# Optimization experiments

Measured on AMD Instinct MI355X. Metric: run time of the kernel, lower is better.

## Reference

```python
import jax, jax.numpy as jnp
import numpy as np

C_M, C_H, C_Z = 256, 32, 128
LN_EPS = 1e-5
MASK_EPS = 1e-8


def setup_inputs() -> dict:
    key = jax.random.key(0)
    ks = jax.random.split(key, 8)
    B, N, L = 1, 128, 256
    m = jax.random.normal(ks[0], (B, N, L, C_M), dtype=jnp.float32)
    msa_mask = jnp.ones((B, N, L), dtype=jnp.float32)
    # parameters
    ln_gamma = jnp.ones((C_M,), dtype=jnp.float32)
    ln_beta = jnp.zeros((C_M,), dtype=jnp.float32)
    sa = 1.0 / np.sqrt(C_M)
    Wa = jax.random.uniform(ks[1], (C_M, C_H), jnp.float32, -sa, sa)
    ba = jax.random.uniform(ks[2], (C_H,), jnp.float32, -sa, sa)
    Wb = jax.random.uniform(ks[3], (C_M, C_H), jnp.float32, -sa, sa)
    bb = jax.random.uniform(ks[4], (C_H,), jnp.float32, -sa, sa)
    so = 1.0 / np.sqrt(C_H * C_H)
    Wo = jax.random.uniform(ks[5], (C_H * C_H, C_Z), jnp.float32, -so, so)
    bo = jax.random.uniform(ks[6], (C_Z,), jnp.float32, -so, so)
    return {"m": m, "msa_mask": msa_mask, "ln_gamma": ln_gamma, "ln_beta": ln_beta,
            "Wa": Wa, "ba": ba, "Wb": Wb, "bb": bb, "Wo": Wo, "bo": bo}


def reference(m, msa_mask, ln_gamma, ln_beta, Wa, ba, Wb, bb, Wo, bo):
    B, N, L, _ = m.shape
    # LayerNorm over c_m
    mu = jnp.mean(m, axis=-1, keepdims=True)
    var = jnp.mean(jnp.square(m - mu), axis=-1, keepdims=True)
    x = (m - mu) * jax.lax.rsqrt(var + LN_EPS) * ln_gamma + ln_beta
    a = x @ Wa + ba                       # [B,N,L,c_h]
    b = x @ Wb + bb                       # [B,N,L,c_h]
    mk = msa_mask[..., None]
    a = a * mk
    b = b * mk
    # outer product mean over MSA depth: [B,L,L,c_h,c_h]
    outer = jnp.einsum('bnic,bnjd->bijcd', a, b)
    pair_mask = jnp.einsum('bni,bnj->bij', msa_mask, msa_mask)
    outer = outer / (pair_mask[..., None, None] + MASK_EPS)
    outer = outer.reshape(B, L, L, -1)    # [B,L,L,c_h*c_h]
    z_update = outer @ Wo + bo            # [B,L,L,c_z]
    return z_update
```

## Files before the change

kernel.cpp:

```cpp
#include <hip/hip_runtime.h>
#include <hip/hip_bf16.h>


typedef __attribute__((ext_vector_type(8))) short bf8_t;
typedef __attribute__((ext_vector_type(4))) float f32x4;

__device__ __forceinline__ unsigned short f2bf(float f) {
    unsigned int u = __float_as_uint(f);
    u += 0x7fffu + ((u >> 16) & 1u);
    return (unsigned short)(u >> 16);
}
__device__ __forceinline__ unsigned int pack2(float a, float b) {
    return (unsigned int)f2bf(a) | ((unsigned int)f2bf(b) << 16);
}

__device__ __forceinline__ void cp16_async(const void* g, void* l) {
    __builtin_amdgcn_global_load_lds(
        (const __attribute__((address_space(1))) unsigned int*)g,
        (__attribute__((address_space(3))) unsigned int*)l, 16, 0, 0);
}

__global__ __launch_bounds__(256) void k_prep(const float* __restrict__ Wa,
                                              const float* __restrict__ Wb,
                                              unsigned short* __restrict__ WTb) {
    int u = blockIdx.x * 256 + threadIdx.x;
    int h = u >> 8, c = u & 255;
    float v = (h < 32) ? Wa[c * 32 + h] : Wb[c * 32 + (h - 32)];
    WTb[u] = f2bf(v);
}

__global__ __launch_bounds__(256) void k_ln_proj(
    const float* __restrict__ gm, const float* __restrict__ gmask,
    const float* __restrict__ gamma, const float* __restrict__ beta,
    const unsigned short* __restrict__ WTb,
    const float* __restrict__ ba, const float* __restrict__ bb,
    const float* __restrict__ Wo,
    unsigned short* __restrict__ aT, unsigned short* __restrict__ bT,
    unsigned short* __restrict__ W2, float* __restrict__ pmr)
{
    const int tid = threadIdx.x;
    const int tail = (int)blockIdx.x - 2048;
    if (tail >= 0) {
        if (tail < 512) {
            int u = tail * 256 + tid;
            int k = u >> 7, z = u & 127;
            int c = k >> 5, d = k & 31;
            int kp = d * 32 + c;
            int dst = (((z >> 4) * 32 + (kp >> 5)) * 16 + (z & 15)) * 32
                      + ((kp >> 3) & 3) * 8 + (kp & 7);
            W2[dst] = f2bf(Wo[u]);
        } else {
            int u = (tail - 512) * 256 + tid;
            int i = u >> 8, j = u & 255;
            float s = 0.f;
            #pragma unroll 8
            for (int n = 0; n < 128; n++)
                s += gmask[n * 256 + i] * gmask[n * 256 + j];
            pmr[u] = 1.f / (s + 1e-8f);
        }
        return;
    }

    __shared__ __align__(16) unsigned short xlb[16 * 256];
    __shared__ float vl[16 * 64];
    const int lane = tid & 63, w = tid >> 6;
    const int l = blockIdx.x & 255, n0 = ((int)blockIdx.x >> 8) << 4;

    const float4 g4  = ((const float4*)gamma)[lane];
    const float4 be4 = ((const float4*)beta)[lane];

    #pragma unroll
    for (int j = 0; j < 4; j++) {
        int row = w * 4 + j;
        int n = n0 + row;
        float4 v = ((const float4*)(gm + ((size_t)n * 256 + l) * 256))[lane];
        float s = v.x + v.y + v.z + v.w;
        float q = v.x * v.x + v.y * v.y + v.z * v.z + v.w * v.w;
        #pragma unroll
        for (int off = 1; off < 64; off <<= 1) {
            s += __shfl_xor(s, off);
            q += __shfl_xor(q, off);
        }
        float mean = s * (1.f / 256.f);
        float var = fmaxf(q * (1.f / 256.f) - mean * mean, 0.f);
        float rstd = rsqrtf(var + 1e-5f);
        float x0 = (v.x - mean) * rstd * g4.x + be4.x;
        float x1 = (v.y - mean) * rstd * g4.y + be4.y;
        float x2 = (v.z - mean) * rstd * g4.z + be4.z;
        float x3 = (v.w - mean) * rstd * g4.w + be4.w;
        int c8s = lane ^ ((row & 7) << 1);
        *(uint2*)((char*)xlb + row * 512 + (c8s << 3)) =
            make_uint2(pack2(x0, x1), pack2(x2, x3));
    }
    __syncthreads();

    const int kg = lane >> 4, r16 = lane & 15;
    const int h = w * 16 + r16;
    f32x4 acc = {0.f, 0.f, 0.f, 0.f};
    #pragma unroll
    for (int ks = 0; ks < 8; ks++) {
        int c8 = ks * 8 + kg * 2;
        bf8_t af = *(const bf8_t*)((char*)xlb + r16 * 512 +
                                   ((c8 ^ ((r16 & 7) << 1)) << 3));
        bf8_t wf = *(const bf8_t*)(WTb + (size_t)h * 256 + ks * 32 + kg * 8);
        acc = __builtin_amdgcn_mfma_f32_16x16x32_bf16(af, wf, acc, 0, 0, 0);
    }
    float bias = (h < 32) ? ba[h] : bb[h - 32];
    #pragma unroll
    for (int r = 0; r < 4; r++) {
        int nrow = kg * 4 + r;
        float mk = gmask[(size_t)(n0 + nrow) * 256 + l];
        vl[nrow * 64 + h] = (acc[r] + bias) * mk;
    }
    __syncthreads();

    if (tid < 128) {
        int row = tid >> 1, half = tid & 1;
        int hh = row & 31;
        unsigned short* dst = (row < 32) ? aT : bT;
        unsigned int pk[4];
        #pragma unroll
        for (int jj = 0; jj < 4; jj++)
            pk[jj] = pack2(vl[(half * 8 + 2 * jj) * 64 + row],
                           vl[(half * 8 + 2 * jj + 1) * 64 + row]);
        *(uint4*)(dst + ((size_t)l * 32 + hh) * 128 + n0 + half * 8) =
            make_uint4(pk[0], pk[1], pk[2], pk[3]);
    }
}

__global__ __launch_bounds__(512, 3) void k_outer(
    const unsigned short* __restrict__ aT, const unsigned short* __restrict__ bT,
    const unsigned short* __restrict__ W2, const float* __restrict__ pmr,
    const float* __restrict__ bo, float* __restrict__ out)
{
    __shared__ __align__(16) char smem[65536];
    const int tid = threadIdx.x, lane = tid & 63, w = tid >> 6;
    const int wr = w >> 1, wc = w & 1;
    const int tj = blockIdx.x & 63, ti = blockIdx.x >> 6;
    const int kg = lane >> 4, r16 = lane & 15;

    f32x4 acc[4][4];
    #pragma unroll
    for (int mt = 0; mt < 4; mt++)
        #pragma unroll
        for (int nt = 0; nt < 4; nt++)
            acc[mt][nt] = (f32x4){0.f, 0.f, 0.f, 0.f};

    const uint4* gA = (const uint4*)(aT + (size_t)ti * 32768);
    const uint4* gB = (const uint4*)(bT + (size_t)tj * 16384);

    #pragma unroll
    for (int half = 0; half < 2; half++) {
        #pragma unroll
        for (int t = 0; t < 4; t++) {
            int q = w * 256 + t * 64 + lane;
            int row = q >> 3, c = q & 7;
            cp16_async(gA + row * 16 + half * 8 + (c ^ (row & 7)),
                       smem + ((w * 256 + t * 64) << 4));
        }
        #pragma unroll
        for (int t = 0; t < 2; t++) {
            int q = w * 128 + t * 64 + lane;
            int row = q >> 3, c = q & 7;
            cp16_async(gB + row * 16 + half * 8 + (c ^ (row & 7)),
                       smem + 32768 + ((w * 128 + t * 64) << 4));
        }
        __syncthreads();

        #pragma unroll
        for (int ks2 = 0; ks2 < 2; ks2++) {
            int ch = ks2 * 4 + kg;
            bf8_t af[4];
            #pragma unroll
            for (int mt = 0; mt < 4; mt++) {
                int mm = wr * 64 + mt * 16 + r16;
                af[mt] = *(const bf8_t*)(smem + mm * 128 + ((ch ^ (mm & 7)) << 4));
            }
            #pragma unroll
            for (int nt = 0; nt < 4; nt++) {
                int nn = wc * 64 + nt * 16 + r16;
                bf8_t bfr = *(const bf8_t*)(smem + 32768 + nn * 128 +
                                            ((ch ^ (nn & 7)) << 4));
                #pragma unroll
                for (int mt = 0; mt < 4; mt++)
                    acc[mt][nt] = __builtin_amdgcn_mfma_f32_16x16x32_bf16(
                        af[mt], bfr, acc[mt][nt], 0, 0, 0);
            }
        }
        __syncthreads();
    }

    unsigned short* O2b = (unsigned short*)smem;
    #pragma unroll
    for (int mt = 0; mt < 4; mt++) {
        int mmb = wr * 64 + mt * 16 + kg * 4;
        #pragma unroll
        for (int nt = 0; nt < 4; nt++) {
            int nn = wc * 64 + nt * 16 + r16;
            int p  = ((mmb >> 5) << 2) | (nn >> 5);
            int k2 = ((nn & 31) << 5) | (mmb & 31);
            int c2 = k2 >> 3;
            int pc = c2 ^ ((c2 >> 3) & 7) ^ (p & 7);
            *(uint2*)(O2b + p * 1024 + pc * 8 + (k2 & 7)) =
                make_uint2(pack2(acc[mt][nt][0], acc[mt][nt][1]),
                           pack2(acc[mt][nt][2], acc[mt][nt][3]));
        }
    }
    __syncthreads();

    f32x4 acc2[2];
    acc2[0] = (f32x4){0.f, 0.f, 0.f, 0.f};
    acc2[1] = (f32x4){0.f, 0.f, 0.f, 0.f};
    const unsigned short* O2r = O2b + r16 * 1024;
    const int psw = r16 & 7;
    const unsigned short* wz = W2 + (size_t)w * 16384 + r16 * 32 + kg * 8;

#define W2LD(x) (*(const bf8_t*)(wz + (x) * 512))
    bf8_t w0 = W2LD(0), w1 = W2LD(1), w2 = W2LD(2), w3 = W2LD(3);
    bf8_t w4 = W2LD(4), w5 = W2LD(5), w6 = W2LD(6), w7 = W2LD(7);

#define S2_ITER(s, wreg, PF)                                                  \
    {                                                                         \
        bf8_t wcur = wreg;                                                    \
        PF;                                                                   \
        int c2 = (s) * 4 + kg;                                                \
        int pc = c2 ^ ((c2 >> 3) & 7) ^ psw;                                  \
        bf8_t a0 = *(const bf8_t*)(O2r + pc * 8);                             \
        bf8_t a1 = *(const bf8_t*)(O2r + 16384 + pc * 8);                     \
        acc2[0] = __builtin_amdgcn_mfma_f32_16x16x32_bf16(a0, wcur, acc2[0],  \
                                                          0, 0, 0);           \
        acc2[1] = __builtin_amdgcn_mfma_f32_16x16x32_bf16(a1, wcur, acc2[1],  \
                                                          0, 0, 0);           \
    }

    #pragma unroll
    for (int sb = 0; sb < 4; sb++) {
        S2_ITER(sb * 8 + 0, w0, if (sb < 3) w0 = W2LD(sb * 8 + 8))
        S2_ITER(sb * 8 + 1, w1, if (sb < 3) w1 = W2LD(sb * 8 + 9))
        S2_ITER(sb * 8 + 2, w2, if (sb < 3) w2 = W2LD(sb * 8 + 10))
        S2_ITER(sb * 8 + 3, w3, if (sb < 3) w3 = W2LD(sb * 8 + 11))
        S2_ITER(sb * 8 + 4, w4, if (sb < 3) w4 = W2LD(sb * 8 + 12))
        S2_ITER(sb * 8 + 5, w5, if (sb < 3) w5 = W2LD(sb * 8 + 13))
        S2_ITER(sb * 8 + 6, w6, if (sb < 3) w6 = W2LD(sb * 8 + 14))
        S2_ITER(sb * 8 + 7, w7, if (sb < 3) w7 = W2LD(sb * 8 + 15))
    }
#undef S2_ITER
#undef W2LD

    const int i0 = ti * 8, j0 = tj * 4;
    const int z = w * 16 + r16;
    const float boz = bo[z];
    #pragma unroll
    for (int mt = 0; mt < 2; mt++)
        #pragma unroll
        for (int r = 0; r < 4; r++) {
            int p = mt * 16 + kg * 4 + r;
            int i = i0 + (p >> 2), j = j0 + (p & 3);
            float recip = pmr[i * 256 + j];
            out[((size_t)(i * 256 + j)) * 128 + z] = acc2[mt][r] * recip + boz;
        }
}

extern "C" void kernel_launch(void* const* d_in, const int* in_sizes, int n_in,
                              void* d_out, int out_size, void* d_ws, size_t ws_size,
                              hipStream_t stream)
{
    const float* m    = (const float*)d_in[0];
    const float* mask = (const float*)d_in[1];
    const float* gam  = (const float*)d_in[2];
    const float* bet  = (const float*)d_in[3];
    const float* Wa   = (const float*)d_in[4];
    const float* ba   = (const float*)d_in[5];
    const float* Wb   = (const float*)d_in[6];
    const float* bb   = (const float*)d_in[7];
    const float* Wo   = (const float*)d_in[8];
    const float* bo   = (const float*)d_in[9];
    float* out = (float*)d_out;

    unsigned short* aT  = (unsigned short*)d_ws;
    unsigned short* bT  = aT + 8192 * 128;
    unsigned short* W2  = bT + 8192 * 128;
    unsigned short* WTb = W2 + 128 * 1024;
    float* pmr = (float*)(WTb + 64 * 256);

    k_prep   <<<  64, 256, 0, stream>>>(Wa, Wb, WTb);
    k_ln_proj<<<2816, 256, 0, stream>>>(m, mask, gam, bet, WTb, ba, bb, Wo,
                                        aT, bT, W2, pmr);
    k_outer  <<<2048, 512, 0, stream>>>(aT, bT, W2, pmr, bo, out);
}
```

Measured before the change: 157.5 us.

## Enlarge outer-product tile to 8x8 residue pairs and split output GEMM by K halves

The k_outer block tile grows from 8x4 to 8x8 residue pairs, halving the grid to 1024 blocks. Each block now loads a full 256-row B tile, and each warp accumulates 8x4 MFMA tiles. Because the larger outer-product result no longer fits in shared memory, it is staged through LDS in two K halves that feed the Wo projection, with an extra barrier between them. This is meant to halve redundant Wo (W2) loads per output and improve reuse, at the cost of doubled accumulator registers and occupancy lowered to 2 blocks per CU.

```diff
diff --git a/kernel.cpp b/kernel.cpp
--- a/kernel.cpp
+++ b/kernel.cpp
@@ -128,26 +128,26 @@
     }
 }
 
-__global__ __launch_bounds__(512, 3) void k_outer(
+__global__ __launch_bounds__(512, 2) void k_outer(
     const unsigned short* __restrict__ aT, const unsigned short* __restrict__ bT,
     const unsigned short* __restrict__ W2, const float* __restrict__ pmr,
     const float* __restrict__ bo, float* __restrict__ out)
 {
     __shared__ __align__(16) char smem[65536];
     const int tid = threadIdx.x, lane = tid & 63, w = tid >> 6;
-    const int wr = w >> 1, wc = w & 1;
-    const int tj = blockIdx.x & 63, ti = blockIdx.x >> 6;
+    const int wr = w >> 2, wc = w & 3;
+    const int tj = blockIdx.x & 31, ti = blockIdx.x >> 5;
     const int kg = lane >> 4, r16 = lane & 15;
 
-    f32x4 acc[4][4];
-    #pragma unroll
-    for (int mt = 0; mt < 4; mt++)
+    f32x4 acc[8][4];
+    #pragma unroll
+    for (int mt = 0; mt < 8; mt++)
         #pragma unroll
         for (int nt = 0; nt < 4; nt++)
             acc[mt][nt] = (f32x4){0.f, 0.f, 0.f, 0.f};
 
     const uint4* gA = (const uint4*)(aT + (size_t)ti * 32768);
-    const uint4* gB = (const uint4*)(bT + (size_t)tj * 16384);
+    const uint4* gB = (const uint4*)(bT + (size_t)tj * 32768);
 
     #pragma unroll
     for (int half = 0; half < 2; half++) {
@@ -156,24 +156,24 @@
             int q = w * 256 + t * 64 + lane;
             int row = q >> 3, c = q & 7;
             cp16_async(gA + row * 16 + half * 8 + (c ^ (row & 7)),
-                       smem + ((w * 256 + t * 64) << 4));
-        }
-        #pragma unroll
-        for (int t = 0; t < 2; t++) {
-            int q = w * 128 + t * 64 + lane;
+                       smem + (q << 4) - (lane << 4));
+        }
+        #pragma unroll
+        for (int t = 0; t < 4; t++) {
+            int q = w * 256 + t * 64 + lane;
             int row = q >> 3, c = q & 7;
             cp16_async(gB + row * 16 + half * 8 + (c ^ (row & 7)),
-                       smem + 32768 + ((w * 128 + t * 64) << 4));
+                       smem + 32768 + (q << 4) - (lane << 4));
         }
         __syncthreads();
 
         #pragma unroll
         for (int ks2 = 0; ks2 < 2; ks2++) {
             int ch = ks2 * 4 + kg;
-            bf8_t af[4];
+            bf8_t af[8];
             #pragma unroll
-            for (int mt = 0; mt < 4; mt++) {
-                int mm = wr * 64 + mt * 16 + r16;
+            for (int mt = 0; mt < 8; mt++) {
+                int mm = wr * 128 + mt * 16 + r16;
                 af[mt] = *(const bf8_t*)(smem + mm * 128 + ((ch ^ (mm & 7)) << 4));
             }
             #pragma unroll
@@ -182,7 +182,7 @@
                 bf8_t bfr = *(const bf8_t*)(smem + 32768 + nn * 128 +
                                             ((ch ^ (nn & 7)) << 4));
                 #pragma unroll
-                for (int mt = 0; mt < 4; mt++)
+                for (int mt = 0; mt < 8; mt++)
                     acc[mt][nt] = __builtin_amdgcn_mfma_f32_16x16x32_bf16(
                         af[mt], bfr, acc[mt][nt], 0, 0, 0);
             }
@@ -191,27 +191,9 @@
     }
 
     unsigned short* O2b = (unsigned short*)smem;
-    #pragma unroll
-    for (int mt = 0; mt < 4; mt++) {
-        int mmb = wr * 64 + mt * 16 + kg * 4;
-        #pragma unroll
-        for (int nt = 0; nt < 4; nt++) {
-            int nn = wc * 64 + nt * 16 + r16;
-            int p  = ((mmb >> 5) << 2) | (nn >> 5);
-            int k2 = ((nn & 31) << 5) | (mmb & 31);
-            int c2 = k2 >> 3;
-            int pc = c2 ^ ((c2 >> 3) & 7) ^ (p & 7);
-            *(uint2*)(O2b + p * 1024 + pc * 8 + (k2 & 7)) =
-                make_uint2(pack2(acc[mt][nt][0], acc[mt][nt][1]),
-                           pack2(acc[mt][nt][2], acc[mt][nt][3]));
-        }
-    }
-    __syncthreads();
-
-    f32x4 acc2[2];
-    acc2[0] = (f32x4){0.f, 0.f, 0.f, 0.f};
-    acc2[1] = (f32x4){0.f, 0.f, 0.f, 0.f};
-    const unsigned short* O2r = O2b + r16 * 1024;
+    f32x4 acc2[4];
+    #pragma unroll
+    for (int q = 0; q < 4; q++) acc2[q] = (f32x4){0.f, 0.f, 0.f, 0.f};
     const int psw = r16 & 7;
     const unsigned short* wz = W2 + (size_t)w * 16384 + r16 * 32 + kg * 8;
 
@@ -219,45 +201,78 @@
     bf8_t w0 = W2LD(0), w1 = W2LD(1), w2 = W2LD(2), w3 = W2LD(3);
     bf8_t w4 = W2LD(4), w5 = W2LD(5), w6 = W2LD(6), w7 = W2LD(7);
 
-#define S2_ITER(s, wreg, PF)                                                  \
+#define S2_ITER(sl, wreg, PF)                                                 \
     {                                                                         \
         bf8_t wcur = wreg;                                                    \
         PF;                                                                   \
-        int c2 = (s) * 4 + kg;                                                \
-        int pc = c2 ^ ((c2 >> 3) & 7) ^ psw;                                  \
-        bf8_t a0 = *(const bf8_t*)(O2r + pc * 8);                             \
-        bf8_t a1 = *(const bf8_t*)(O2r + 16384 + pc * 8);                     \
+        int c2h = (sl) * 4 + kg;                                              \
+        int pcs = c2h ^ ((c2h >> 3) & 7) ^ psw;                               \
+        const unsigned short* ar = O2b + r16 * 512 + pcs * 8;                 \
+        bf8_t a0 = *(const bf8_t*)(ar);                                       \
+        bf8_t a1 = *(const bf8_t*)(ar + 16 * 512);                            \
+        bf8_t a2 = *(const bf8_t*)(ar + 32 * 512);                            \
+        bf8_t a3 = *(const bf8_t*)(ar + 48 * 512);                            \
         acc2[0] = __builtin_amdgcn_mfma_f32_16x16x32_bf16(a0, wcur, acc2[0],  \
                                                           0, 0, 0);           \
         acc2[1] = __builtin_amdgcn_mfma_f32_16x16x32_bf16(a1, wcur, acc2[1],  \
                                                           0, 0, 0);           \
-    }
-
-    #pragma unroll
-    for (int sb = 0; sb < 4; sb++) {
-        S2_ITER(sb * 8 + 0, w0, if (sb < 3) w0 = W2LD(sb * 8 + 8))
-        S2_ITER(sb * 8 + 1, w1, if (sb < 3) w1 = W2LD(sb * 8 + 9))
-        S2_ITER(sb * 8 + 2, w2, if (sb < 3) w2 = W2LD(sb * 8 + 10))
-        S2_ITER(sb * 8 + 3, w3, if (sb < 3) w3 = W2LD(sb * 8 + 11))
-        S2_ITER(sb * 8 + 4, w4, if (sb < 3) w4 = W2LD(sb * 8 + 12))
-        S2_ITER(sb * 8 + 5, w5, if (sb < 3) w5 = W2LD(sb * 8 + 13))
-        S2_ITER(sb * 8 + 6, w6, if (sb < 3) w6 = W2LD(sb * 8 + 14))
-        S2_ITER(sb * 8 + 7, w7, if (sb < 3) w7 = W2LD(sb * 8 + 15))
+        acc2[2] = __builtin_amdgcn_mfma_f32_16x16x32_bf16(a2, wcur, acc2[2],  \
+                                                          0, 0, 0);           \
+        acc2[3] = __builtin_amdgcn_mfma_f32_16x16x32_bf16(a3, wcur, acc2[3],  \
+                                                          0, 0, 0);           \
+    }
+
+    #pragma unroll
+    for (int kh = 0; kh < 2; kh++) {
+        if (kh) __syncthreads();
+
+        #pragma unroll
+        for (int mt = 0; mt < 8; mt++) {
+            #pragma unroll
+            for (int ntt = 0; ntt < 2; ntt++) {
+                int nt = ntt * 2 + kh;
+                int p  = (wr * 4 + (mt >> 1)) * 8 + (wc * 2 + ntt);
+                int k2h = r16 * 32 + ((mt & 1) << 4) + kg * 4;
+                int c2h = k2h >> 3;
+                int pcs = c2h ^ ((c2h >> 3) & 7) ^ (p & 7);
+                *(uint2*)(O2b + p * 512 + pcs * 8 + (k2h & 7)) =
+                    make_uint2(pack2(acc[mt][nt][0], acc[mt][nt][1]),
+                               pack2(acc[mt][nt][2], acc[mt][nt][3]));
+            }
+        }
+        __syncthreads();
+
+        S2_ITER(0,  w0, if (kh == 0 || 0  < 8) w0 = W2LD(kh * 16 + 8))
+        S2_ITER(1,  w1, if (kh == 0 || 1  < 8) w1 = W2LD(kh * 16 + 9))
+        S2_ITER(2,  w2, if (kh == 0 || 2  < 8) w2 = W2LD(kh * 16 + 10))
+        S2_ITER(3,  w3, if (kh == 0 || 3  < 8) w3 = W2LD(kh * 16 + 11))
+        S2_ITER(4,  w4, if (kh == 0 || 4  < 8) w4 = W2LD(kh * 16 + 12))
+        S2_ITER(5,  w5, if (kh == 0 || 5  < 8) w5 = W2LD(kh * 16 + 13))
+        S2_ITER(6,  w6, if (kh == 0 || 6  < 8) w6 = W2LD(kh * 16 + 14))
+        S2_ITER(7,  w7, if (kh == 0 || 7  < 8) w7 = W2LD(kh * 16 + 15))
+        S2_ITER(8,  w0, if (kh == 0) w0 = W2LD(16))
+        S2_ITER(9,  w1, if (kh == 0) w1 = W2LD(17))
+        S2_ITER(10, w2, if (kh == 0) w2 = W2LD(18))
+        S2_ITER(11, w3, if (kh == 0) w3 = W2LD(19))
+        S2_ITER(12, w4, if (kh == 0) w4 = W2LD(20))
+        S2_ITER(13, w5, if (kh == 0) w5 = W2LD(21))
+        S2_ITER(14, w6, if (kh == 0) w6 = W2LD(22))
+        S2_ITER(15, w7, if (kh == 0) w7 = W2LD(23))
     }
 #undef S2_ITER
 #undef W2LD
 
-    const int i0 = ti * 8, j0 = tj * 4;
+    const int i0 = ti * 8, j0 = tj * 8;
     const int z = w * 16 + r16;
     const float boz = bo[z];
     #pragma unroll
-    for (int mt = 0; mt < 2; mt++)
+    for (int q = 0; q < 4; q++)
         #pragma unroll
         for (int r = 0; r < 4; r++) {
-            int p = mt * 16 + kg * 4 + r;
-            int i = i0 + (p >> 2), j = j0 + (p & 3);
+            int p = q * 16 + kg * 4 + r;
+            int i = i0 + (p >> 3), j = j0 + (p & 7);
             float recip = pmr[i * 256 + j];
-            out[((size_t)(i * 256 + j)) * 128 + z] = acc2[mt][r] * recip + boz;
+            out[((size_t)(i * 256 + j)) * 128 + z] = acc2[q][r] * recip + boz;
         }
 }
 
@@ -286,5 +301,5 @@
     k_prep   <<<  64, 256, 0, stream>>>(Wa, Wb, WTb);
     k_ln_proj<<<2816, 256, 0, stream>>>(m, mask, gam, bet, WTb, ba, bb, Wo,
                                         aT, bT, W2, pmr);
-    k_outer  <<<2048, 512, 0, stream>>>(aT, bT, W2, pmr, bo, out);
-}
+    k_outer  <<<1024, 512, 0, stream>>>(aT, bT, W2, pmr, bo, out);
+}
```

Result: no change. 159.0 us, median of 2 (+1.0%).
